# Kernel tuning notes

Hardware: AMD Instinct MI355X
Metric: run time of the kernel (lower is better)

The kernel has to match this reference:

```python
import jax, jax.numpy as jnp
import numpy as np

E = 1_000_000
NODE_IN = 64
EDGE_IN = 32
GLOBAL_IN = 32
HIDDEN = 128
EDGE_OUT = 32
B = 128


def setup_inputs() -> dict:
    key = jax.random.key(0)
    ks = jax.random.split(key, 10)
    src = jax.random.normal(ks[0], (E, NODE_IN), dtype=jnp.float32)
    dest = jax.random.normal(ks[1], (E, NODE_IN), dtype=jnp.float32)
    edge_attr = jax.random.normal(ks[2], (E, EDGE_IN), dtype=jnp.float32)
    u = jax.random.normal(ks[3], (B, GLOBAL_IN), dtype=jnp.float32)
    edge_batch = jnp.sort(jax.random.randint(ks[4], (E,), 0, B, dtype=jnp.int32)).astype(jnp.int64)
    in_dim = EDGE_IN + 2 * NODE_IN + GLOBAL_IN  # 192
    # Kaiming-uniform-ish init scale, values irrelevant for correctness baseline
    W1 = jax.random.normal(ks[5], (in_dim, HIDDEN), dtype=jnp.float32) * (1.0 / np.sqrt(in_dim))
    b1 = jnp.zeros((HIDDEN,), dtype=jnp.float32)
    W2 = jax.random.normal(ks[6], (HIDDEN, EDGE_OUT), dtype=jnp.float32) * (1.0 / np.sqrt(HIDDEN))
    b2 = jnp.zeros((EDGE_OUT,), dtype=jnp.float32)
    return {"src": src, "dest": dest, "edge_attr": edge_attr, "u": u,
            "edge_batch": edge_batch, "W1": W1, "b1": b1, "W2": W2, "b2": b2}


def reference(src, dest, edge_attr, u, edge_batch, W1, b1, W2, b2):
    # gather per-edge global features: [E, global_in_dim]
    u_expanded = u[edge_batch]
    # concat -> [E, edge_in + 2*node_in + global_in]
    combined = jnp.concatenate([src, dest, edge_attr, u_expanded], axis=1)
    # 2-layer MLP with ReLU
    h = jax.nn.relu(combined @ W1 + b1)
    out = h @ W2 + b2
    return out
```

## Files before the change

kernel.cpp:

```cpp
#include <hip/hip_runtime.h>

#define NODE_IN 64
#define EDGE_IN 32
#define GLOBAL_IN 32
#define HID 128
#define EOUT 32

typedef float f32x4 __attribute__((ext_vector_type(4)));
typedef float f32x2 __attribute__((ext_vector_type(2)));
typedef short s16x8 __attribute__((ext_vector_type(8)));
typedef unsigned short u16x8 __attribute__((ext_vector_type(8)));

__device__ __forceinline__ unsigned short f2bf(float f) {
  __bf16 h = (__bf16)f;
  return __builtin_bit_cast(unsigned short, h);
}

__device__ __forceinline__ void stage8(const float* __restrict__ p,
                                       unsigned short* dst) {
  const f32x4 a = *(const f32x4*)p;
  const f32x4 b = *(const f32x4*)(p + 4);
  u16x8 v = { f2bf(a[0]), f2bf(a[1]), f2bf(a[2]), f2bf(a[3]),
              f2bf(b[0]), f2bf(b[1]), f2bf(b[2]), f2bf(b[3]) };
  *(u16x8*)dst = v;
}

__global__ __launch_bounds__(256) void edge_mlp(
    const float* __restrict__ srcp, const float* __restrict__ dstp,
    const float* __restrict__ eap, const float* __restrict__ up,
    const int* __restrict__ ebp, const float* __restrict__ W1,
    const float* __restrict__ b1, const float* __restrict__ W2,
    const float* __restrict__ b2, float* __restrict__ outp,
    int E, int ntiles)
{
  __shared__ __align__(16) unsigned short SM[64 * 200];

  const int t = threadIdx.x;
  const int wid = t >> 6;
  const int lane = t & 63;
  const int g = lane >> 4;
  const int r16 = lane & 15;

  s16x8 w1f[6][2];
#pragma unroll
  for (int kk = 0; kk < 6; ++kk) {
#pragma unroll
    for (int nt = 0; nt < 2; ++nt) {
      s16x8 v;
#pragma unroll
      for (int j = 0; j < 8; ++j)
        v[j] = (short)f2bf(W1[(32*kk + 8*g + j)*HID + 32*wid + 2*r16 + nt]);
      w1f[kk][nt] = v;
    }
  }
  s16x8 w2f[4][2];
#pragma unroll
  for (int kk = 0; kk < 4; ++kk) {
#pragma unroll
    for (int nt = 0; nt < 2; ++nt) {
      s16x8 v;
#pragma unroll
      for (int j = 0; j < 8; ++j)
        v[j] = (short)f2bf(W2[(32*kk + 8*g + j)*EOUT + 2*r16 + nt]);
      w2f[kk][nt] = v;
    }
  }
  const float b1v0 = b1[32*wid + 2*r16];
  const float b1v1 = b1[32*wid + 2*r16 + 1];
  const float b2v0 = b2[2*r16];
  const float b2v1 = b2[2*r16 + 1];

  for (int tile = blockIdx.x; tile < ntiles; tile += gridDim.x) {
    const int mbase = tile * 64;

#pragma unroll
    for (int k = 0; k < 2; ++k) {
      const int cid = t + 256*k;
      const int row = cid >> 3, c = cid & 7;
      const int grow = min(mbase + row, E - 1);
      stage8(srcp + (size_t)grow*NODE_IN + 8*c, &SM[row*200 + 8*c]);
    }
#pragma unroll
    for (int k = 0; k < 2; ++k) {
      const int cid = t + 256*k;
      const int row = cid >> 3, c = cid & 7;
      const int grow = min(mbase + row, E - 1);
      stage8(dstp + (size_t)grow*NODE_IN + 8*c, &SM[row*200 + 64 + 8*c]);
    }
    {
      const int row = t >> 2, c = t & 3;
      const int grow = min(mbase + row, E - 1);
      stage8(eap + (size_t)grow*EDGE_IN + 8*c, &SM[row*200 + 128 + 8*c]);
      const int bb = ebp[grow];
      stage8(up + (size_t)bb*GLOBAL_IN + 8*c, &SM[row*200 + 160 + 8*c]);
    }
    __syncthreads();

    f32x4 acc[4][2];
    {
      const f32x4 z = {0.f, 0.f, 0.f, 0.f};
#pragma unroll
      for (int mi = 0; mi < 4; ++mi) { acc[mi][0] = z; acc[mi][1] = z; }
    }
#pragma unroll
    for (int kk = 0; kk < 6; ++kk) {
#pragma unroll
      for (int mi = 0; mi < 4; ++mi) {
        const s16x8 a = *(const s16x8*)&SM[(16*mi + r16)*200 + 32*kk + 8*g];
        acc[mi][0] = __builtin_amdgcn_mfma_f32_16x16x32_bf16(a, w1f[kk][0], acc[mi][0], 0, 0, 0);
        acc[mi][1] = __builtin_amdgcn_mfma_f32_16x16x32_bf16(a, w1f[kk][1], acc[mi][1], 0, 0, 0);
      }
    }
    __syncthreads();

#pragma unroll
    for (int mi = 0; mi < 4; ++mi) {
#pragma unroll
      for (int j = 0; j < 4; ++j) {
        const float h0 = fmaxf(acc[mi][0][j] + b1v0, 0.f);
        const float h1 = fmaxf(acc[mi][1][j] + b1v1, 0.f);
        const unsigned int pk = (unsigned int)f2bf(h0) |
                                ((unsigned int)f2bf(h1) << 16);
        *(unsigned int*)&SM[(16*mi + 4*g + j)*136 + 32*wid + 2*r16] = pk;
      }
    }
    __syncthreads();

    f32x4 acc2[2];
    {
      const f32x4 z = {0.f, 0.f, 0.f, 0.f};
      acc2[0] = z; acc2[1] = z;
    }
#pragma unroll
    for (int kk = 0; kk < 4; ++kk) {
      const s16x8 a = *(const s16x8*)&SM[(16*wid + r16)*136 + 32*kk + 8*g];
      acc2[0] = __builtin_amdgcn_mfma_f32_16x16x32_bf16(a, w2f[kk][0], acc2[0], 0, 0, 0);
      acc2[1] = __builtin_amdgcn_mfma_f32_16x16x32_bf16(a, w2f[kk][1], acc2[1], 0, 0, 0);
    }
#pragma unroll
    for (int j = 0; j < 4; ++j) {
      const int m = mbase + 16*wid + 4*g + j;
      if (m < E) {
        f32x2 o = { acc2[0][j] + b2v0, acc2[1][j] + b2v1 };
        *(f32x2*)(outp + (size_t)m*EOUT + 2*r16) = o;
      }
    }
    __syncthreads();
  }
}

extern "C" void kernel_launch(void* const* d_in, const int* in_sizes, int n_in,
                              void* d_out, int out_size, void* d_ws, size_t ws_size,
                              hipStream_t stream) {
  const float* srcp = (const float*)d_in[0];
  const float* dstp = (const float*)d_in[1];
  const float* eap  = (const float*)d_in[2];
  const float* up   = (const float*)d_in[3];
  const int*   ebp  = (const int*)d_in[4];
  const float* W1   = (const float*)d_in[5];
  const float* b1   = (const float*)d_in[6];
  const float* W2   = (const float*)d_in[7];
  const float* b2   = (const float*)d_in[8];
  float* outp = (float*)d_out;

  const int E = in_sizes[0] / NODE_IN;
  const int ntiles = (E + 63) / 64;
  const int grid = ntiles < 2048 ? ntiles : 2048;

  edge_mlp<<<grid, 256, 0, stream>>>(srcp, dstp, eap, up, ebp, W1, b1, W2, b2,
                                     outp, E, ntiles);
}
```

Before: 164.1 us.

## Load MFMA A-fragments directly from global and double-buffer hidden tile

Drops the shared-memory staging of the concatenated input rows. Each wave now loads its bf16 A-fragments for the first-layer MFMAs straight from global memory, with the batch-index gather done per row. The hidden-activation buffer is double-buffered, which removes two of the three block-wide barriers per tile and is meant to improve latency hiding in this bandwidth-bound kernel. In exchange, all four waves load the same 64 input rows, so L1/L2 request traffic roughly quadruples, and the per-lane 32-byte segments are less coalesced than the old staging loads.

```diff
diff --git a/kernel.cpp b/kernel.cpp
--- a/kernel.cpp
+++ b/kernel.cpp
@@ -16,13 +16,12 @@
   return __builtin_bit_cast(unsigned short, h);
 }
 
-__device__ __forceinline__ void stage8(const float* __restrict__ p,
-                                       unsigned short* dst) {
+__device__ __forceinline__ s16x8 ld_frag(const float* __restrict__ p) {
   const f32x4 a = *(const f32x4*)p;
   const f32x4 b = *(const f32x4*)(p + 4);
   u16x8 v = { f2bf(a[0]), f2bf(a[1]), f2bf(a[2]), f2bf(a[3]),
               f2bf(b[0]), f2bf(b[1]), f2bf(b[2]), f2bf(b[3]) };
-  *(u16x8*)dst = v;
+  return __builtin_bit_cast(s16x8, v);
 }
 
 __global__ __launch_bounds__(256) void edge_mlp(
@@ -33,7 +32,7 @@
     const float* __restrict__ b2, float* __restrict__ outp,
     int E, int ntiles)
 {
-  __shared__ __align__(16) unsigned short SM[64 * 200];
+  __shared__ __align__(16) unsigned short Hb[2][64 * 136];
 
   const int t = threadIdx.x;
   const int wid = t >> 6;
@@ -69,32 +68,16 @@
   const float b1v1 = b1[32*wid + 2*r16 + 1];
   const float b2v0 = b2[2*r16];
   const float b2v1 = b2[2*r16 + 1];
+  const int Em1 = E - 1;
 
-  for (int tile = blockIdx.x; tile < ntiles; tile += gridDim.x) {
+  int buf = 0;
+  for (int tile = blockIdx.x; tile < ntiles; tile += gridDim.x, buf ^= 1) {
     const int mbase = tile * 64;
 
+    int bb[4];
 #pragma unroll
-    for (int k = 0; k < 2; ++k) {
-      const int cid = t + 256*k;
-      const int row = cid >> 3, c = cid & 7;
-      const int grow = min(mbase + row, E - 1);
-      stage8(srcp + (size_t)grow*NODE_IN + 8*c, &SM[row*200 + 8*c]);
-    }
-#pragma unroll
-    for (int k = 0; k < 2; ++k) {
-      const int cid = t + 256*k;
-      const int row = cid >> 3, c = cid & 7;
-      const int grow = min(mbase + row, E - 1);
-      stage8(dstp + (size_t)grow*NODE_IN + 8*c, &SM[row*200 + 64 + 8*c]);
-    }
-    {
-      const int row = t >> 2, c = t & 3;
-      const int grow = min(mbase + row, E - 1);
-      stage8(eap + (size_t)grow*EDGE_IN + 8*c, &SM[row*200 + 128 + 8*c]);
-      const int bb = ebp[grow];
-      stage8(up + (size_t)bb*GLOBAL_IN + 8*c, &SM[row*200 + 160 + 8*c]);
-    }
-    __syncthreads();
+    for (int mi = 0; mi < 4; ++mi)
+      bb[mi] = ebp[min(mbase + 16*mi + r16, Em1)];
 
     f32x4 acc[4][2];
     {
@@ -103,16 +86,31 @@
       for (int mi = 0; mi < 4; ++mi) { acc[mi][0] = z; acc[mi][1] = z; }
     }
 #pragma unroll
-    for (int kk = 0; kk < 6; ++kk) {
-#pragma unroll
-      for (int mi = 0; mi < 4; ++mi) {
-        const s16x8 a = *(const s16x8*)&SM[(16*mi + r16)*200 + 32*kk + 8*g];
-        acc[mi][0] = __builtin_amdgcn_mfma_f32_16x16x32_bf16(a, w1f[kk][0], acc[mi][0], 0, 0, 0);
-        acc[mi][1] = __builtin_amdgcn_mfma_f32_16x16x32_bf16(a, w1f[kk][1], acc[mi][1], 0, 0, 0);
-      }
+    for (int mi = 0; mi < 4; ++mi) {
+      const int row = min(mbase + 16*mi + r16, Em1);
+      const float* ps = srcp + (size_t)row*NODE_IN + 8*g;
+      const float* pd = dstp + (size_t)row*NODE_IN + 8*g;
+      const s16x8 f0 = ld_frag(ps);
+      const s16x8 f1 = ld_frag(ps + 32);
+      const s16x8 f2 = ld_frag(pd);
+      const s16x8 f3 = ld_frag(pd + 32);
+      const s16x8 f4 = ld_frag(eap + (size_t)row*EDGE_IN + 8*g);
+      const s16x8 f5 = ld_frag(up + (size_t)bb[mi]*GLOBAL_IN + 8*g);
+      acc[mi][0] = __builtin_amdgcn_mfma_f32_16x16x32_bf16(f0, w1f[0][0], acc[mi][0], 0, 0, 0);
+      acc[mi][1] = __builtin_amdgcn_mfma_f32_16x16x32_bf16(f0, w1f[0][1], acc[mi][1], 0, 0, 0);
+      acc[mi][0] = __builtin_amdgcn_mfma_f32_16x16x32_bf16(f1, w1f[1][0], acc[mi][0], 0, 0, 0);
+      acc[mi][1] = __builtin_amdgcn_mfma_f32_16x16x32_bf16(f1, w1f[1][1], acc[mi][1], 0, 0, 0);
+      acc[mi][0] = __builtin_amdgcn_mfma_f32_16x16x32_bf16(f2, w1f[2][0], acc[mi][0], 0, 0, 0);
+      acc[mi][1] = __builtin_amdgcn_mfma_f32_16x16x32_bf16(f2, w1f[2][1], acc[mi][1], 0, 0, 0);
+      acc[mi][0] = __builtin_amdgcn_mfma_f32_16x16x32_bf16(f3, w1f[3][0], acc[mi][0], 0, 0, 0);
+      acc[mi][1] = __builtin_amdgcn_mfma_f32_16x16x32_bf16(f3, w1f[3][1], acc[mi][1], 0, 0, 0);
+      acc[mi][0] = __builtin_amdgcn_mfma_f32_16x16x32_bf16(f4, w1f[4][0], acc[mi][0], 0, 0, 0);
+      acc[mi][1] = __builtin_amdgcn_mfma_f32_16x16x32_bf16(f4, w1f[4][1], acc[mi][1], 0, 0, 0);
+      acc[mi][0] = __builtin_amdgcn_mfma_f32_16x16x32_bf16(f5, w1f[5][0], acc[mi][0], 0, 0, 0);
+      acc[mi][1] = __builtin_amdgcn_mfma_f32_16x16x32_bf16(f5, w1f[5][1], acc[mi][1], 0, 0, 0);
     }
-    __syncthreads();
 
+    unsigned short* __restrict__ H = &Hb[buf][0];
 #pragma unroll
     for (int mi = 0; mi < 4; ++mi) {
 #pragma unroll
@@ -121,7 +119,7 @@
         const float h1 = fmaxf(acc[mi][1][j] + b1v1, 0.f);
         const unsigned int pk = (unsigned int)f2bf(h0) |
                                 ((unsigned int)f2bf(h1) << 16);
-        *(unsigned int*)&SM[(16*mi + 4*g + j)*136 + 32*wid + 2*r16] = pk;
+        *(unsigned int*)&H[(16*mi + 4*g + j)*136 + 32*wid + 2*r16] = pk;
       }
     }
     __syncthreads();
@@ -133,7 +131,7 @@
     }
 #pragma unroll
     for (int kk = 0; kk < 4; ++kk) {
-      const s16x8 a = *(const s16x8*)&SM[(16*wid + r16)*136 + 32*kk + 8*g];
+      const s16x8 a = *(const s16x8*)&H[(16*wid + r16)*136 + 32*kk + 8*g];
       acc2[0] = __builtin_amdgcn_mfma_f32_16x16x32_bf16(a, w2f[kk][0], acc2[0], 0, 0, 0);
       acc2[1] = __builtin_amdgcn_mfma_f32_16x16x32_bf16(a, w2f[kk][1], acc2[1], 0, 0, 0);
     }
@@ -145,7 +143,6 @@
         *(f32x2*)(outp + (size_t)m*EOUT + 2*r16) = o;
       }
     }
-    __syncthreads();
   }
 }
 
```

Result: slower. 340.8 us (+107.7%).

## Software-pipeline global loads through registers and split LDS buffers for X and H

Applied to the files above, without the earlier changes.

Tile loads are prefetched into registers two tiles ahead, and the edge_batch index three tiles ahead, so global memory latency overlaps the MFMA work of the current tile. Input and hidden activations get separate LDS buffers, which lets the kernel drop two of the four block barriers per tile. The remaining barriers become a custom lgkmcnt wait plus s_barrier rather than __syncthreads. This costs extra VGPRs (48 floats of prefetch state) and may lower occupancy.

```diff
diff --git a/kernel.cpp b/kernel.cpp
--- a/kernel.cpp
+++ b/kernel.cpp
@@ -16,13 +16,16 @@
   return __builtin_bit_cast(unsigned short, h);
 }
 
-__device__ __forceinline__ void stage8(const float* __restrict__ p,
-                                       unsigned short* dst) {
-  const f32x4 a = *(const f32x4*)p;
-  const f32x4 b = *(const f32x4*)(p + 4);
+__device__ __forceinline__ u16x8 cvt8(f32x4 a, f32x4 b) {
   u16x8 v = { f2bf(a[0]), f2bf(a[1]), f2bf(a[2]), f2bf(a[3]),
               f2bf(b[0]), f2bf(b[1]), f2bf(b[2]), f2bf(b[3]) };
-  *(u16x8*)dst = v;
+  return v;
+}
+
+__device__ __forceinline__ void bar_lds() {
+  asm volatile("s_waitcnt lgkmcnt(0)" ::: "memory");
+  __builtin_amdgcn_s_barrier();
+  asm volatile("" ::: "memory");
 }
 
 __global__ __launch_bounds__(256) void edge_mlp(
@@ -33,13 +36,19 @@
     const float* __restrict__ b2, float* __restrict__ outp,
     int E, int ntiles)
 {
-  __shared__ __align__(16) unsigned short SM[64 * 200];
+  __shared__ __align__(16) unsigned short SMX[64 * 200];
+  __shared__ __align__(16) unsigned short SMH[64 * 136];
 
   const int t = threadIdx.x;
   const int wid = t >> 6;
   const int lane = t & 63;
   const int g = lane >> 4;
   const int r16 = lane & 15;
+  const int rA = t >> 3;
+  const int cA = (t & 7) * 8;
+  const int rC = t >> 2;
+  const int cC = (t & 3) * 8;
+  const int Em1 = E - 1;
 
   s16x8 w1f[6][2];
 #pragma unroll
@@ -70,31 +79,54 @@
   const float b2v0 = b2[2*r16];
   const float b2v1 = b2[2*r16 + 1];
 
-  for (int tile = blockIdx.x; tile < ntiles; tile += gridDim.x) {
+  f32x4 P[12];
+  auto issue_sde = [&](int mb) {
+    const int r0 = min(mb + rA, Em1);
+    const int r1 = min(mb + 32 + rA, Em1);
+    const int r2 = min(mb + rC, Em1);
+    const float* s0 = srcp + (size_t)r0 * NODE_IN + cA;
+    const float* s1 = srcp + (size_t)r1 * NODE_IN + cA;
+    const float* d0 = dstp + (size_t)r0 * NODE_IN + cA;
+    const float* d1 = dstp + (size_t)r1 * NODE_IN + cA;
+    const float* e0 = eap  + (size_t)r2 * EDGE_IN + cC;
+    P[0] = *(const f32x4*)s0;  P[1] = *(const f32x4*)(s0 + 4);
+    P[2] = *(const f32x4*)s1;  P[3] = *(const f32x4*)(s1 + 4);
+    P[4] = *(const f32x4*)d0;  P[5] = *(const f32x4*)(d0 + 4);
+    P[6] = *(const f32x4*)d1;  P[7] = *(const f32x4*)(d1 + 4);
+    P[8] = *(const f32x4*)e0;  P[9] = *(const f32x4*)(e0 + 4);
+  };
+  auto issue_u = [&](int bb) {
+    const float* uu = up + (size_t)bb * GLOBAL_IN + cC;
+    P[10] = *(const f32x4*)uu;  P[11] = *(const f32x4*)(uu + 4);
+  };
+  auto write_x = [&]() {
+    *(u16x8*)&SMX[rA*200 + cA]           = cvt8(P[0], P[1]);
+    *(u16x8*)&SMX[(rA+32)*200 + cA]      = cvt8(P[2], P[3]);
+    *(u16x8*)&SMX[rA*200 + 64 + cA]      = cvt8(P[4], P[5]);
+    *(u16x8*)&SMX[(rA+32)*200 + 64 + cA] = cvt8(P[6], P[7]);
+    *(u16x8*)&SMX[rC*200 + 128 + cC]     = cvt8(P[8], P[9]);
+    *(u16x8*)&SMX[rC*200 + 160 + cC]     = cvt8(P[10], P[11]);
+  };
+
+  int tile = blockIdx.x;
+  const int TS = gridDim.x;
+
+  {
+    const int mb0 = tile * 64;
+    const int eb0 = ebp[min(mb0 + rC, Em1)];
+    issue_sde(mb0);
+    issue_u(eb0);
+    write_x();
+    const int mb1 = (tile + TS) * 64;
+    const int eb1 = ebp[min(mb1 + rC, Em1)];
+    issue_sde(mb1);
+    issue_u(eb1);
+  }
+  int ebv = ebp[min((tile + 2*TS) * 64 + rC, Em1)];
+  bar_lds();
+
+  for (; tile < ntiles; tile += TS) {
     const int mbase = tile * 64;
-
-#pragma unroll
-    for (int k = 0; k < 2; ++k) {
-      const int cid = t + 256*k;
-      const int row = cid >> 3, c = cid & 7;
-      const int grow = min(mbase + row, E - 1);
-      stage8(srcp + (size_t)grow*NODE_IN + 8*c, &SM[row*200 + 8*c]);
-    }
-#pragma unroll
-    for (int k = 0; k < 2; ++k) {
-      const int cid = t + 256*k;
-      const int row = cid >> 3, c = cid & 7;
-      const int grow = min(mbase + row, E - 1);
-      stage8(dstp + (size_t)grow*NODE_IN + 8*c, &SM[row*200 + 64 + 8*c]);
-    }
-    {
-      const int row = t >> 2, c = t & 3;
-      const int grow = min(mbase + row, E - 1);
-      stage8(eap + (size_t)grow*EDGE_IN + 8*c, &SM[row*200 + 128 + 8*c]);
-      const int bb = ebp[grow];
-      stage8(up + (size_t)bb*GLOBAL_IN + 8*c, &SM[row*200 + 160 + 8*c]);
-    }
-    __syncthreads();
 
     f32x4 acc[4][2];
     {
@@ -106,12 +138,11 @@
     for (int kk = 0; kk < 6; ++kk) {
 #pragma unroll
       for (int mi = 0; mi < 4; ++mi) {
-        const s16x8 a = *(const s16x8*)&SM[(16*mi + r16)*200 + 32*kk + 8*g];
+        const s16x8 a = *(const s16x8*)&SMX[(16*mi + r16)*200 + 32*kk + 8*g];
         acc[mi][0] = __builtin_amdgcn_mfma_f32_16x16x32_bf16(a, w1f[kk][0], acc[mi][0], 0, 0, 0);
         acc[mi][1] = __builtin_amdgcn_mfma_f32_16x16x32_bf16(a, w1f[kk][1], acc[mi][1], 0, 0, 0);
       }
     }
-    __syncthreads();
 
 #pragma unroll
     for (int mi = 0; mi < 4; ++mi) {
@@ -121,10 +152,10 @@
         const float h1 = fmaxf(acc[mi][1][j] + b1v1, 0.f);
         const unsigned int pk = (unsigned int)f2bf(h0) |
                                 ((unsigned int)f2bf(h1) << 16);
-        *(unsigned int*)&SM[(16*mi + 4*g + j)*136 + 32*wid + 2*r16] = pk;
+        *(unsigned int*)&SMH[(16*mi + 4*g + j)*136 + 32*wid + 2*r16] = pk;
       }
     }
-    __syncthreads();
+    bar_lds();
 
     f32x4 acc2[2];
     {
@@ -133,7 +164,7 @@
     }
 #pragma unroll
     for (int kk = 0; kk < 4; ++kk) {
-      const s16x8 a = *(const s16x8*)&SM[(16*wid + r16)*136 + 32*kk + 8*g];
+      const s16x8 a = *(const s16x8*)&SMH[(16*wid + r16)*136 + 32*kk + 8*g];
       acc2[0] = __builtin_amdgcn_mfma_f32_16x16x32_bf16(a, w2f[kk][0], acc2[0], 0, 0, 0);
       acc2[1] = __builtin_amdgcn_mfma_f32_16x16x32_bf16(a, w2f[kk][1], acc2[1], 0, 0, 0);
     }
@@ -145,7 +176,12 @@
         *(f32x2*)(outp + (size_t)m*EOUT + 2*r16) = o;
       }
     }
-    __syncthreads();
+
+    write_x();
+    issue_sde((tile + 2*TS) * 64);
+    issue_u(ebv);
+    ebv = ebp[min((tile + 3*TS) * 64 + rC, Em1)];
+    bar_lds();
   }
 }
 
```

After: 155.1 us. -5.5%, faster.
